# Optimization experiments

Measured on AMD Instinct MI355X. Metric: run time of the kernel, lower is better.

Reference implementation:

```python
import jax, jax.numpy as jnp
import numpy as np

B, N, D, H, HID = 8, 512, 512, 8, 2048


def setup_inputs() -> dict:
    key = jax.random.key(0)
    ks = jax.random.split(key, 8)
    s = 0.02
    p = lambda i, shape: jax.random.normal(ks[i], shape, jnp.float32) * s
    return dict(
        x=jax.random.normal(ks[0], (B, N, D), jnp.float32),
        Wq=p(1, (D, D)), bq=jnp.zeros((D,), jnp.float32),
        Wk=p(2, (D, D)), bk=jnp.zeros((D,), jnp.float32),
        Wv=p(3, (D, D)), bv=jnp.zeros((D,), jnp.float32),
        Wsig=p(4, (H, D)), bsig=jnp.zeros((H,), jnp.float32),
        ln1_g=jnp.ones((D,), jnp.float32), ln1_b=jnp.zeros((D,), jnp.float32),
        W1=p(5, (HID, D)), b1=jnp.zeros((HID,), jnp.float32),
        W2=p(6, (D, HID)), b2=jnp.zeros((D,), jnp.float32),
        ln2_g=jnp.ones((D,), jnp.float32), ln2_b=jnp.zeros((D,), jnp.float32),
    )


def _ln(z, g, b, eps=1e-5):
    m = jnp.mean(z, axis=-1, keepdims=True)
    v = jnp.var(z, axis=-1, keepdims=True)
    return (z - m) * jax.lax.rsqrt(v + eps) * g + b


def reference(x, Wq, bq, Wk, bk, Wv, bv, Wsig, bsig,
              ln1_g, ln1_b, W1, b1, W2, b2, ln2_g, ln2_b):
    Bb, Nn, Dd = x.shape
    Hh = bsig.shape[0]
    dh = Dd // Hh
    # --- AnomalyAttention: series attention S, Gaussian prior P, Z = S @ V ---
    Q = (x @ Wq.T + bq).reshape(Bb, Nn, Hh, dh)
    K = (x @ Wk.T + bk).reshape(Bb, Nn, Hh, dh)
    V = (x @ Wv.T + bv).reshape(Bb, Nn, Hh, dh)
    scores = jnp.einsum('bnhd,bmhd->bhnm', Q, K) / jnp.sqrt(jnp.float32(dh))
    S = jax.nn.softmax(scores, axis=-1)                       # [B,H,N,N]
    # learned positive scale sigma per (batch, position, head)
    sigma = jax.nn.softplus(x @ Wsig.T + bsig) + 1e-5         # [B,N,H]
    idx = jnp.arange(Nn, dtype=jnp.float32)
    dist2 = (idx[:, None] - idx[None, :]) ** 2                # [N,N]
    sig = jnp.transpose(sigma, (0, 2, 1))[..., None]          # [B,H,N,1]
    gauss = jnp.exp(-dist2 / (2.0 * sig * sig)) / (jnp.sqrt(2.0 * jnp.pi) * sig)
    P = gauss / jnp.sum(gauss, axis=-1, keepdims=True)        # row-normalized prior
    Zh = jnp.einsum('bhnm,bmhd->bnhd', S, V).reshape(Bb, Nn, Dd)
    # --- residual + LayerNorm + MLP(relu) + residual + LayerNorm ---
    Z = _ln(Zh + x, ln1_g, ln1_b)
    hidden = jax.nn.relu(Z @ W1.T + b1)
    x_hat = hidden @ W2.T + b2
    x_hat = _ln(x_hat + Z, ln2_g, ln2_b)
    return (x_hat, P, S)
```

## Files before the change

### kernel.cpp

```cpp
#include <hip/hip_runtime.h>
#include <cstdint>

typedef short s16x8 __attribute__((ext_vector_type(8)));
typedef float f32x4 __attribute__((ext_vector_type(4)));
using u16 = unsigned short;


__device__ __forceinline__ u16 f2bf(float f) {
    union { float f; uint32_t u; } v; v.f = f;
    uint32_t u = v.u;
    return (u16)((u + 0x7FFFu + ((u >> 16) & 1u)) >> 16);
}

__device__ __forceinline__ void gload_lds16(const void* g, void* l) {
    __builtin_amdgcn_global_load_lds(
        (const __attribute__((address_space(1))) unsigned int*)g,
        (__attribute__((address_space(3))) unsigned int*)l, 16, 0, 0);
}

__device__ __forceinline__ s16x8 pack_bf8(f32x4 a, f32x4 b) {
    union { s16x8 s; uint32_t w[4]; } o;
    uint32_t a0 = __float_as_uint(a[0]), a1 = __float_as_uint(a[1]);
    uint32_t a2 = __float_as_uint(a[2]), a3 = __float_as_uint(a[3]);
    uint32_t b0 = __float_as_uint(b[0]), b1 = __float_as_uint(b[1]);
    uint32_t b2 = __float_as_uint(b[2]), b3 = __float_as_uint(b[3]);
    o.w[0] = (a0 >> 16) | (a1 & 0xffff0000u);
    o.w[1] = (a2 >> 16) | (a3 & 0xffff0000u);
    o.w[2] = (b0 >> 16) | (b1 & 0xffff0000u);
    o.w[3] = (b2 >> 16) | (b3 & 0xffff0000u);
    return o.s;
}

__global__ __launch_bounds__(256) void k_convert_sigma(
    const float* __restrict__ x, const float* __restrict__ wq,
    const float* __restrict__ wk, const float* __restrict__ wv,
    const float* __restrict__ w1, const float* __restrict__ w2,
    const float* __restrict__ bq, const float* __restrict__ bk,
    const float* __restrict__ bv,
    const float* __restrict__ Wsig, const float* __restrict__ bsig,
    u16* __restrict__ xb, u16* __restrict__ wqb, u16* __restrict__ wkb,
    u16* __restrict__ wvb, u16* __restrict__ w1b, u16* __restrict__ w2b,
    float* __restrict__ biascat, float* __restrict__ sigT)
{
    int bk_ = blockIdx.x;
    int tid = threadIdx.x;
    if (bk_ >= 4866) {
        int row  = (int)(((bk_ - 4866) * 256 + tid) >> 6);
        int lane = tid & 63;
        const float4* xr = (const float4*)(x + (long)row * 512);
        float4 xa = xr[lane * 2], xc = xr[lane * 2 + 1];
        float xs[8] = {xa.x, xa.y, xa.z, xa.w, xc.x, xc.y, xc.z, xc.w};
        float ph[8];
#pragma unroll
        for (int h = 0; h < 8; ++h) {
            const float4* wr = (const float4*)(Wsig + h * 512);
            float4 wa = wr[lane * 2], wc = wr[lane * 2 + 1];
            ph[h] = xs[0]*wa.x + xs[1]*wa.y + xs[2]*wa.z + xs[3]*wa.w
                  + xs[4]*wc.x + xs[5]*wc.y + xs[6]*wc.z + xs[7]*wc.w;
        }
#pragma unroll
        for (int h = 0; h < 8; ++h)
#pragma unroll
            for (int m = 1; m < 64; m <<= 1)
                ph[h] += __shfl_xor(ph[h], m, 64);
        if (lane < 8) {
            float z  = ph[lane] + bsig[lane];
            float sp = fmaxf(z, 0.f) + log1pf(__expf(-fabsf(z)));
            int b = row >> 9, n = row & 511;
            sigT[(((long)b * 8 + lane) << 9) + n] = sp + 1e-5f;
        }
        return;
    }
    long g = (long)bk_ * 256 + tid;
    if (g >= 1245184) {
        long id = g - 1245184;
        if (id < 384) {
            const float* src = id < 128 ? bq : id < 256 ? bk : bv;
            ((float4*)biascat)[id] = ((const float4*)src)[id & 127];
        }
        return;
    }
    const float* src; u16* dst; long off;
    if      (g <  524288) { src = x;  dst = xb;  off = g; }
    else if (g <  589824) { src = wq; dst = wqb; off = g -  524288; }
    else if (g <  655360) { src = wk; dst = wkb; off = g -  589824; }
    else if (g <  720896) { src = wv; dst = wvb; off = g -  655360; }
    else if (g <  983040) { src = w1; dst = w1b; off = g -  720896; }
    else                  { src = w2; dst = w2b; off = g -  983040; }
    float4 v = ((const float4*)src)[off];
    ushort4 o;
    o.x = f2bf(v.x); o.y = f2bf(v.y); o.z = f2bf(v.z); o.w = f2bf(v.w);
    ((ushort4*)dst)[off] = o;
}

template<int BM, int BN, int EPI>
__global__ __launch_bounds__(512) void k_gemm_nt(
    const u16* __restrict__ A, const u16* __restrict__ B,
    const float* __restrict__ bias, void* __restrict__ C,
    int lda, int ldb, int K)
{
    constexpr int BK = 64;
    __shared__ __align__(16) u16 As[2][BM * BK];
    __shared__ __align__(16) u16 Bs[2][BN * BK];

    const u16* Ag = A + (long)blockIdx.x * BM * lda;
    const u16* Bg = B + (long)blockIdx.y * BN * ldb;

    int tid  = threadIdx.x;
    int wave = tid >> 6, lane = tid & 63;
    int wm = wave >> 2, wn = wave & 3;
    constexpr int WTM = BM / 2, WTN = BN / 4;
    constexpr int FM = WTM / 16, FN = WTN / 16;
    int r16 = lane & 15, g4 = lane >> 4;

    f32x4 acc[FM][FN];
#pragma unroll
    for (int i = 0; i < FM; ++i)
#pragma unroll
        for (int j = 0; j < FN; ++j) acc[i][j] = (f32x4){0.f, 0.f, 0.f, 0.f};

    constexpr int nA = BM * BK / (512 * 8);
    constexpr int nB = BN * BK / (512 * 8);

    auto stage = [&](int buf, int k0) {
#pragma unroll
        for (int c = 0; c < nA; ++c) {
            int e = c * 512 + tid;
            int r = e >> 3, s = e & 7;
            gload_lds16(Ag + (long)r * lda + k0 + ((s ^ (r & 7)) * 8),
                        &As[buf][e * 8]);
        }
#pragma unroll
        for (int c = 0; c < nB; ++c) {
            int e = c * 512 + tid;
            int r = e >> 3, s = e & 7;
            gload_lds16(Bg + (long)r * ldb + k0 + ((s ^ (r & 7)) * 8),
                        &Bs[buf][e * 8]);
        }
    };

    stage(0, 0);
    __syncthreads();
    int cur = 0;
    const int NT = K / BK;
    for (int t = 0; t < NT; ++t) {
        if (t + 1 < NT) stage(cur ^ 1, (t + 1) * BK);
#pragma unroll
        for (int kk = 0; kk < 2; ++kk) {
            s16x8 af[FM], bfr[FN];
#pragma unroll
            for (int fm = 0; fm < FM; ++fm) {
                int row = wm * WTM + fm * 16 + r16;
                int slot = (kk * 4 + g4) ^ (row & 7);
                af[fm] = *(const s16x8*)&As[cur][row * 64 + slot * 8];
            }
#pragma unroll
            for (int fn = 0; fn < FN; ++fn) {
                int row = wn * WTN + fn * 16 + r16;
                int slot = (kk * 4 + g4) ^ (row & 7);
                bfr[fn] = *(const s16x8*)&Bs[cur][row * 64 + slot * 8];
            }
#pragma unroll
            for (int fm = 0; fm < FM; ++fm)
#pragma unroll
                for (int fn = 0; fn < FN; ++fn)
                    acc[fm][fn] = __builtin_amdgcn_mfma_f32_16x16x32_bf16(af[fm], bfr[fn], acc[fm][fn], 0, 0, 0);
        }
        __syncthreads();
        cur ^= 1;
    }

    int i0 = blockIdx.x * BM + wm * WTM;
    int j0 = blockIdx.y * BN + wn * WTN;
#pragma unroll
    for (int fm = 0; fm < FM; ++fm)
#pragma unroll
        for (int fn = 0; fn < FN; ++fn)
#pragma unroll
            for (int j = 0; j < 4; ++j) {
                int gi = i0 + fm * 16 + (g4 << 2) + j;
                int gj = j0 + fn * 16 + r16;
                float v = acc[fm][fn][j];
                if constexpr (EPI == 3) {
                    v = fmaxf(v + bias[gj], 0.f);
                    ((u16*)C)[(long)gi * 2048 + gj] = f2bf(v);
                } else if constexpr (EPI == 4) {
                    ((float*)C)[(long)gi * 512 + gj] = v + bias[gj];
                } else {
                    v += bias[gj];
                    int mat = gj >> 9, cj = gj & 511;
                    int h = cj >> 6, d = cj & 63, b = gi >> 9, n = gi & 511;
                    u16* base = (u16*)C;
                    if (mat == 0)
                        base[(((long)(b * 8 + h) * 512 + n) << 6) + d] = f2bf(v);
                    else if (mat == 1)
                        (base + 2097152)[(((long)(b * 8 + h) * 512 + n) << 6) + d] = f2bf(v);
                    else
                        (base + 4194304)[(((long)(b * 8 + h) * 64 + d) << 9) + n] = f2bf(v);
                }
            }
}

__global__ __launch_bounds__(256) void k_attn_pv(
    const u16* __restrict__ Qb, const u16* __restrict__ Kb,
    const u16* __restrict__ Vt, const float* __restrict__ sigT,
    float* __restrict__ S, float* __restrict__ Zh, float* __restrict__ P)
{
    __shared__ float Sb[4][16][260];
    int bh = blockIdx.y;
    int rb = blockIdx.x;
    int tid = threadIdx.x;
    int wave = tid >> 6, lane = tid & 63;
    int r16 = lane & 15, g4 = lane >> 4, hi8 = g4 * 8;

    const u16* Qg = Qb + ((long)bh * 512 + rb * 64 + wave * 16) * 64;
    const u16* Kg = Kb + (long)bh * 512 * 64;
    const u16* Vg = Vt + (long)bh * 64 * 512;

    s16x8 qa[2];
    qa[0] = *(const s16x8*)(Qg + r16 * 64 + hi8);
    qa[1] = *(const s16x8*)(Qg + r16 * 64 + 32 + hi8);

    f32x4 acc[32];
#pragma unroll
    for (int t = 0; t < 32; ++t) acc[t] = (f32x4){0.f, 0.f, 0.f, 0.f};

#pragma unroll
    for (int ch = 0; ch < 4; ++ch)
#pragma unroll
        for (int kk = 0; kk < 2; ++kk)
#pragma unroll
            for (int fn = 0; fn < 8; ++fn) {
                s16x8 b = *(const s16x8*)(Kg + (long)(ch * 128 + fn * 16 + r16) * 64 + kk * 32 + hi8);
                acc[ch * 8 + fn] = __builtin_amdgcn_mfma_f32_16x16x32_bf16(qa[kk], b, acc[ch * 8 + fn], 0, 0, 0);
            }

    float mx[4] = {-1e30f, -1e30f, -1e30f, -1e30f};
#pragma unroll
    for (int t = 0; t < 32; ++t)
#pragma unroll
        for (int j = 0; j < 4; ++j) mx[j] = fmaxf(mx[j], acc[t][j]);
#pragma unroll
    for (int j = 0; j < 4; ++j)
#pragma unroll
        for (int m = 1; m < 16; m <<= 1) mx[j] = fmaxf(mx[j], __shfl_xor(mx[j], m, 64));

    float sum[4] = {0.f, 0.f, 0.f, 0.f};
#pragma unroll
    for (int t = 0; t < 32; ++t)
#pragma unroll
        for (int j = 0; j < 4; ++j) {
            float p = __expf(0.125f * (acc[t][j] - mx[j]));
            acc[t][j] = p;
            sum[j] += p;
        }
#pragma unroll
    for (int j = 0; j < 4; ++j) {
#pragma unroll
        for (int m = 1; m < 16; m <<= 1) sum[j] += __shfl_xor(sum[j], m, 64);
        sum[j] = 1.0f / sum[j];
    }
#pragma unroll
    for (int t = 0; t < 32; ++t)
#pragma unroll
        for (int j = 0; j < 4; ++j) acc[t][j] *= sum[j];

    long sbase = ((long)bh * 512 + rb * 64 + wave * 16) * 512;
#pragma unroll
    for (int t = 0; t < 32; ++t) {
        int col = t * 16 + r16;
#pragma unroll
        for (int j = 0; j < 4; ++j)
            S[sbase + (long)(g4 * 4 + j) * 512 + col] = acc[t][j];
    }

    f32x4 zacc[4];
#pragma unroll
    for (int fn = 0; fn < 4; ++fn) zacc[fn] = (f32x4){0.f, 0.f, 0.f, 0.f};

#pragma unroll
    for (int p = 0; p < 2; ++p) {
#pragma unroll
        for (int t = 0; t < 16; ++t)
#pragma unroll
            for (int j = 0; j < 4; ++j)
                Sb[wave][g4 * 4 + j][t * 16 + r16] = acc[p * 16 + t][j];
#pragma unroll
        for (int kk = 0; kk < 8; ++kk) {
            f32x4 lo = *(const f32x4*)&Sb[wave][r16][kk * 32 + hi8];
            f32x4 hi = *(const f32x4*)&Sb[wave][r16][kk * 32 + hi8 + 4];
            s16x8 pa = pack_bf8(lo, hi);
#pragma unroll
            for (int fn = 0; fn < 4; ++fn) {
                s16x8 vb = *(const s16x8*)(Vg + (long)(fn * 16 + r16) * 512 + p * 256 + kk * 32 + hi8);
                zacc[fn] = __builtin_amdgcn_mfma_f32_16x16x32_bf16(pa, vb, zacc[fn], 0, 0, 0);
            }
        }
    }

    long zb = ((long)(bh >> 3) * 512 + rb * 64 + wave * 16) * 512 + (bh & 7) * 64;
#pragma unroll
    for (int fn = 0; fn < 4; ++fn)
#pragma unroll
        for (int j = 0; j < 4; ++j)
            Zh[zb + (long)(g4 * 4 + j) * 512 + fn * 16 + r16] = zacc[fn][j];

    const float* sig = sigT + (long)bh * 512 + rb * 64 + wave * 16;
    long pbase = ((long)bh * 512 + rb * 64 + wave * 16) * 512;
#pragma unroll
    for (int rr = 0; rr < 16; ++rr) {
        float s = sig[rr];
        float a = -1.0f / (2.0f * s * s);
        int n = rb * 64 + wave * 16 + rr;
        float e[8]; float sum2 = 0.f;
#pragma unroll
        for (int j = 0; j < 8; ++j) {
            float d = (float)(n - (lane * 8 + j));
            e[j] = __expf(a * d * d);
            sum2 += e[j];
        }
#pragma unroll
        for (int m = 1; m < 64; m <<= 1) sum2 += __shfl_xor(sum2, m, 64);
        float r = 1.0f / sum2;
        float4* dst = (float4*)(P + pbase + (long)rr * 512 + lane * 8);
        dst[0] = make_float4(e[0]*r, e[1]*r, e[2]*r, e[3]*r);
        dst[1] = make_float4(e[4]*r, e[5]*r, e[6]*r, e[7]*r);
    }
}

template<bool WBF>
__global__ __launch_bounds__(256) void k_ln(
    const float* __restrict__ a, const float* __restrict__ b,
    const float* __restrict__ g, const float* __restrict__ bt,
    float* __restrict__ y, u16* __restrict__ yb)
{
    int row  = (int)((blockIdx.x * 256 + threadIdx.x) >> 6);
    int lane = threadIdx.x & 63;
    const float4* ar = (const float4*)(a + (long)row * 512);
    const float4* br = (const float4*)(b + (long)row * 512);
    float4 a0 = ar[lane * 2], a1 = ar[lane * 2 + 1];
    float4 b0 = br[lane * 2], b1 = br[lane * 2 + 1];
    float v[8] = {a0.x + b0.x, a0.y + b0.y, a0.z + b0.z, a0.w + b0.w,
                  a1.x + b1.x, a1.y + b1.y, a1.z + b1.z, a1.w + b1.w};
    float s = 0.f, q = 0.f;
#pragma unroll
    for (int j = 0; j < 8; ++j) { s += v[j]; q += v[j] * v[j]; }
#pragma unroll
    for (int m = 1; m < 64; m <<= 1) {
        s += __shfl_xor(s, m, 64);
        q += __shfl_xor(q, m, 64);
    }
    float mean = s * (1.f / 512.f);
    float var  = q * (1.f / 512.f) - mean * mean;
    float rstd = rsqrtf(var + 1e-5f);
    const float4* gr = (const float4*)(g + lane * 8);
    const float4* tr = (const float4*)(bt + lane * 8);
    float4 g0 = gr[0], g1 = gr[1], t0 = tr[0], t1 = tr[1];
    float gg[8] = {g0.x, g0.y, g0.z, g0.w, g1.x, g1.y, g1.z, g1.w};
    float tt[8] = {t0.x, t0.y, t0.z, t0.w, t1.x, t1.y, t1.z, t1.w};
    float o[8];
#pragma unroll
    for (int j = 0; j < 8; ++j) o[j] = (v[j] - mean) * rstd * gg[j] + tt[j];
    float4* yr = (float4*)(y + (long)row * 512 + lane * 8);
    yr[0] = make_float4(o[0], o[1], o[2], o[3]);
    yr[1] = make_float4(o[4], o[5], o[6], o[7]);
    if constexpr (WBF) {
        s16x8 ob;
#pragma unroll
        for (int j = 0; j < 8; ++j) ob[j] = (short)f2bf(o[j]);
        *(s16x8*)(yb + (long)row * 512 + lane * 8) = ob;
    }
}

extern "C" void kernel_launch(void* const* d_in, const int* in_sizes, int n_in,
                              void* d_out, int out_size, void* d_ws, size_t ws_size,
                              hipStream_t stream)
{
    const float* x    = (const float*)d_in[0];
    const float* Wq   = (const float*)d_in[1];
    const float* bq   = (const float*)d_in[2];
    const float* Wk   = (const float*)d_in[3];
    const float* bk   = (const float*)d_in[4];
    const float* Wv   = (const float*)d_in[5];
    const float* bv   = (const float*)d_in[6];
    const float* Wsig = (const float*)d_in[7];
    const float* bsig = (const float*)d_in[8];
    const float* g1   = (const float*)d_in[9];
    const float* be1  = (const float*)d_in[10];
    const float* W1   = (const float*)d_in[11];
    const float* b1   = (const float*)d_in[12];
    const float* W2   = (const float*)d_in[13];
    const float* b2   = (const float*)d_in[14];
    const float* g2   = (const float*)d_in[15];
    const float* be2  = (const float*)d_in[16];

    float* out_xhat = (float*)d_out;
    float* out_P    = out_xhat + 2097152;
    float* out_S    = out_P + 16777216;

    char* ws = (char*)d_ws;
    u16*   xb   = (u16*)(ws + 0);
    u16*   Qb   = (u16*)(ws + 4194304);
    u16*   hid  = (u16*)(ws + 0);
    u16*   Wqb  = (u16*)(ws + 16777216);
    u16*   W1b  = (u16*)(ws + 18350080);
    u16*   W2b  = (u16*)(ws + 20447232);
    float* sigT = (float*)(ws + 22544384);
    float* Zh   = (float*)(ws + 22675456);
    float* bcat = (float*)(ws + 22675456);
    float* x2   = (float*)(ws + 22675456);
    float* Z    = (float*)(ws + 31064064);
    u16*   Zb   = (u16*)(ws + 39452672);

    u16* Wkb = Wqb + 262144;
    u16* Wvb = Wqb + 524288;

    k_convert_sigma<<<5890, 256, 0, stream>>>(x, Wq, Wk, Wv, W1, W2, bq, bk, bv,
                                              Wsig, bsig,
                                              xb, Wqb, Wkb, Wvb, W1b, W2b,
                                              bcat, sigT);

    k_gemm_nt<128,128,5><<<dim3(32,12,1),512,0,stream>>>(
        xb, Wqb, bcat, Qb, 512, 512, 512);

    k_attn_pv<<<dim3(8,64),256,0,stream>>>(Qb, Qb + 2097152, Qb + 4194304,
                                           sigT, out_S, Zh, out_P);

    k_ln<true><<<1024,256,0,stream>>>(Zh, x, g1, be1, Z, Zb);

    k_gemm_nt<128,128,3><<<dim3(32,16,1),512,0,stream>>>(Zb, W1b, b1, hid, 512, 512, 512);

    k_gemm_nt<64,128,4><<<dim3(64,4,1),512,0,stream>>>(hid, W2b, b2, x2, 2048, 2048, 2048);

    k_ln<false><<<1024,256,0,stream>>>(x2, Z, g2, be2, out_xhat, nullptr);
}
```

Before: 140.9 us.

## Retune GEMM to 256 threads, coalesce nontemporal S/P stores, add MFMA priority

The GEMM kernel drops from 512 to 256 threads per block. Each wave now computes a larger tile, K becomes a compile-time constant and the k-loop is fully unrolled. In the attention kernel, S is written through the existing LDS staging buffer as coalesced float4 nontemporal stores instead of scattered scalar stores, and P also uses nontemporal stores. s_setprio brackets the MFMA sections. The aim is better store coalescing and less cache pollution, at the cost of fewer waves per GEMM block, more register pressure and larger unrolled code.

Result: slower. 168.0 us (+19.2%).

```diff
diff --git a/kernel.cpp b/kernel.cpp
--- a/kernel.cpp
+++ b/kernel.cpp
@@ -16,6 +16,10 @@
     __builtin_amdgcn_global_load_lds(
         (const __attribute__((address_space(1))) unsigned int*)g,
         (__attribute__((address_space(3))) unsigned int*)l, 16, 0, 0);
+}
+
+__device__ __forceinline__ void stnt4(float* p, f32x4 v) {
+    __builtin_nontemporal_store(v, (f32x4*)p);
 }
 
 __device__ __forceinline__ s16x8 pack_bf8(f32x4 a, f32x4 b) {
@@ -93,11 +97,11 @@
     ((ushort4*)dst)[off] = o;
 }
 
-template<int BM, int BN, int EPI>
-__global__ __launch_bounds__(512) void k_gemm_nt(
+template<int BM, int BN, int K, int EPI>
+__global__ __launch_bounds__(256, 2) void k_gemm_nt(
     const u16* __restrict__ A, const u16* __restrict__ B,
     const float* __restrict__ bias, void* __restrict__ C,
-    int lda, int ldb, int K)
+    int lda, int ldb)
 {
     constexpr int BK = 64;
     __shared__ __align__(16) u16 As[2][BM * BK];
@@ -108,8 +112,8 @@
 
     int tid  = threadIdx.x;
     int wave = tid >> 6, lane = tid & 63;
-    int wm = wave >> 2, wn = wave & 3;
-    constexpr int WTM = BM / 2, WTN = BN / 4;
+    int wm = wave >> 1, wn = wave & 1;
+    constexpr int WTM = BM / 2, WTN = BN / 2;
     constexpr int FM = WTM / 16, FN = WTN / 16;
     int r16 = lane & 15, g4 = lane >> 4;
 
@@ -119,20 +123,20 @@
 #pragma unroll
         for (int j = 0; j < FN; ++j) acc[i][j] = (f32x4){0.f, 0.f, 0.f, 0.f};
 
-    constexpr int nA = BM * BK / (512 * 8);
-    constexpr int nB = BN * BK / (512 * 8);
+    constexpr int nA = BM * BK / (256 * 8);
+    constexpr int nB = BN * BK / (256 * 8);
 
     auto stage = [&](int buf, int k0) {
 #pragma unroll
         for (int c = 0; c < nA; ++c) {
-            int e = c * 512 + tid;
+            int e = c * 256 + tid;
             int r = e >> 3, s = e & 7;
             gload_lds16(Ag + (long)r * lda + k0 + ((s ^ (r & 7)) * 8),
                         &As[buf][e * 8]);
         }
 #pragma unroll
         for (int c = 0; c < nB; ++c) {
-            int e = c * 512 + tid;
+            int e = c * 256 + tid;
             int r = e >> 3, s = e & 7;
             gload_lds16(Bg + (long)r * ldb + k0 + ((s ^ (r & 7)) * 8),
                         &Bs[buf][e * 8]);
@@ -142,7 +146,8 @@
     stage(0, 0);
     __syncthreads();
     int cur = 0;
-    const int NT = K / BK;
+    constexpr int NT = K / BK;
+#pragma unroll
     for (int t = 0; t < NT; ++t) {
         if (t + 1 < NT) stage(cur ^ 1, (t + 1) * BK);
 #pragma unroll
@@ -225,6 +230,7 @@
 #pragma unroll
     for (int t = 0; t < 32; ++t) acc[t] = (f32x4){0.f, 0.f, 0.f, 0.f};
 
+    __builtin_amdgcn_s_setprio(1);
 #pragma unroll
     for (int ch = 0; ch < 4; ++ch)
 #pragma unroll
@@ -234,6 +240,7 @@
                 s16x8 b = *(const s16x8*)(Kg + (long)(ch * 128 + fn * 16 + r16) * 64 + kk * 32 + hi8);
                 acc[ch * 8 + fn] = __builtin_amdgcn_mfma_f32_16x16x32_bf16(qa[kk], b, acc[ch * 8 + fn], 0, 0, 0);
             }
+    __builtin_amdgcn_s_setprio(0);
 
     float mx[4] = {-1e30f, -1e30f, -1e30f, -1e30f};
 #pragma unroll
@@ -265,18 +272,11 @@
 #pragma unroll
         for (int j = 0; j < 4; ++j) acc[t][j] *= sum[j];
 
+    f32x4 zacc[4];
+#pragma unroll
+    for (int fn = 0; fn < 4; ++fn) zacc[fn] = (f32x4){0.f, 0.f, 0.f, 0.f};
+
     long sbase = ((long)bh * 512 + rb * 64 + wave * 16) * 512;
-#pragma unroll
-    for (int t = 0; t < 32; ++t) {
-        int col = t * 16 + r16;
-#pragma unroll
-        for (int j = 0; j < 4; ++j)
-            S[sbase + (long)(g4 * 4 + j) * 512 + col] = acc[t][j];
-    }
-
-    f32x4 zacc[4];
-#pragma unroll
-    for (int fn = 0; fn < 4; ++fn) zacc[fn] = (f32x4){0.f, 0.f, 0.f, 0.f};
 
 #pragma unroll
     for (int p = 0; p < 2; ++p) {
@@ -285,6 +285,14 @@
 #pragma unroll
             for (int j = 0; j < 4; ++j)
                 Sb[wave][g4 * 4 + j][t * 16 + r16] = acc[p * 16 + t][j];
+
+#pragma unroll
+        for (int row = 0; row < 16; ++row) {
+            f32x4 sv = *(const f32x4*)&Sb[wave][row][lane * 4];
+            stnt4(&S[sbase + (long)row * 512 + p * 256 + lane * 4], sv);
+        }
+
+        __builtin_amdgcn_s_setprio(1);
 #pragma unroll
         for (int kk = 0; kk < 8; ++kk) {
             f32x4 lo = *(const f32x4*)&Sb[wave][r16][kk * 32 + hi8];
@@ -296,6 +304,7 @@
                 zacc[fn] = __builtin_amdgcn_mfma_f32_16x16x32_bf16(pa, vb, zacc[fn], 0, 0, 0);
             }
         }
+        __builtin_amdgcn_s_setprio(0);
     }
 
     long zb = ((long)(bh >> 3) * 512 + rb * 64 + wave * 16) * 512 + (bh & 7) * 64;
@@ -322,9 +331,9 @@
 #pragma unroll
         for (int m = 1; m < 64; m <<= 1) sum2 += __shfl_xor(sum2, m, 64);
         float r = 1.0f / sum2;
-        float4* dst = (float4*)(P + pbase + (long)rr * 512 + lane * 8);
-        dst[0] = make_float4(e[0]*r, e[1]*r, e[2]*r, e[3]*r);
-        dst[1] = make_float4(e[4]*r, e[5]*r, e[6]*r, e[7]*r);
+        float* dst = P + pbase + (long)rr * 512 + lane * 8;
+        stnt4(dst,     (f32x4){e[0]*r, e[1]*r, e[2]*r, e[3]*r});
+        stnt4(dst + 4, (f32x4){e[4]*r, e[5]*r, e[6]*r, e[7]*r});
     }
 }
 
@@ -420,17 +429,17 @@
                                               xb, Wqb, Wkb, Wvb, W1b, W2b,
                                               bcat, sigT);
 
-    k_gemm_nt<128,128,5><<<dim3(32,12,1),512,0,stream>>>(
-        xb, Wqb, bcat, Qb, 512, 512, 512);
+    k_gemm_nt<128,128,512,5><<<dim3(32,12,1),256,0,stream>>>(
+        xb, Wqb, bcat, Qb, 512, 512);
 
     k_attn_pv<<<dim3(8,64),256,0,stream>>>(Qb, Qb + 2097152, Qb + 4194304,
                                            sigT, out_S, Zh, out_P);
 
     k_ln<true><<<1024,256,0,stream>>>(Zh, x, g1, be1, Z, Zb);
 
-    k_gemm_nt<128,128,3><<<dim3(32,16,1),512,0,stream>>>(Zb, W1b, b1, hid, 512, 512, 512);
-
-    k_gemm_nt<64,128,4><<<dim3(64,4,1),512,0,stream>>>(hid, W2b, b2, x2, 2048, 2048, 2048);
+    k_gemm_nt<128,128,512,3><<<dim3(32,16,1),256,0,stream>>>(Zb, W1b, b1, hid, 512, 512);
+
+    k_gemm_nt<64,128,2048,4><<<dim3(64,4,1),256,0,stream>>>(hid, W2b, b2, x2, 2048, 2048);
 
     k_ln<false><<<1024,256,0,stream>>>(x2, Z, g2, be2, out_xhat, nullptr);
 }
```
